# Kernel tuning notes

Measured on AMD Instinct MI355X. Metric: run time of the kernel, lower is better.

The kernel has to match this reference:

```python
import jax, jax.numpy as jnp
import numpy as np

ALPHA = 3.0
NITERS = 15
POWER_ITERS = 20
ROOTS = [np.cos(np.pi * (2 * i + 1) / (2 * NITERS)) for i in range(NITERS)]


def batch_conv2d(inputs, kernels):
    # inputs: [B,1,H,W], kernels: [B,1,3,3]; per-sample 3x3 stencil via grouped conv
    B, _, H, W = inputs.shape
    out = jax.lax.conv_general_dilated(
        inputs.reshape(1, B, H, W), kernels,
        window_strides=(1, 1), padding=((1, 1), (1, 1)),
        feature_group_count=B,
        dimension_numbers=("NCHW", "OIHW", "NCHW"))
    return out.reshape(B, 1, H, W)


def setup_inputs() -> dict:
    key = jax.random.key(0)
    k1, k2, k3, k4 = jax.random.split(key, 4)
    B, H, W = 64, 512, 512
    x = jax.random.normal(k1, (B, 1, H, W), dtype=jnp.float32)
    f = jax.random.normal(k2, (B, 1, H, W), dtype=jnp.float32)
    kernelA = jax.random.normal(k3, (B, 1, 3, 3), dtype=jnp.float32)
    u = jax.random.normal(k4, (B, 1, H, W), dtype=jnp.float32)
    return {"x": x, "f": f, "kernelA": kernelA, "u": u}


def reference(x, f, kernelA, u):
    # Power iteration to estimate the dominant eigenvalue magnitude m per sample
    for _ in range(POWER_ITERS):
        y = batch_conv2d(u, kernelA)
        m = jnp.max(jnp.abs(y), axis=(2, 3), keepdims=True)  # [B,1,1,1]
        u = y / m
    # Chebyshev step sizes over the band [m/alpha, m]
    taus = jnp.stack(
        [2.0 / (m + m / ALPHA - (m / ALPHA - m) * r) for r in ROOTS])  # [niters,B,1,1,1]

    def cheby_step(xc, tau):
        Ax = batch_conv2d(xc, kernelA)
        return xc + tau * (f - Ax), None

    x, _ = jax.lax.scan(cheby_step, x, taus)
    return x
```

## Files before the change

kernel.cpp:

```cpp
#include <hip/hip_runtime.h>

#define BB 64
#define HH 512
#define WW 512
#define PLANE (HH * WW)
#define N_CHEBY 15
#define FD 5
#define RR 32
#define NS (HH / RR)

struct F8 { float v[8]; };

__device__ __forceinline__ float wshr1(float x) {
    return __int_as_float(__builtin_amdgcn_update_dpp(
        0, __float_as_int(x), 0x138, 0xF, 0xF, true));
}
__device__ __forceinline__ float wshl1(float x) {
    return __int_as_float(__builtin_amdgcn_update_dpp(
        0, __float_as_int(x), 0x130, 0xF, 0xF, true));
}

__device__ __forceinline__ F8 ldrow(const float* plane, int y, int lane, bool ok) {
    F8 r;
    if (ok) {
        const float4* p =
            reinterpret_cast<const float4*>(plane + (size_t)y * WW + (lane << 3));
        const float4 a = p[0], b = p[1];
        r.v[0] = a.x; r.v[1] = a.y; r.v[2] = a.z; r.v[3] = a.w;
        r.v[4] = b.x; r.v[5] = b.y; r.v[6] = b.z; r.v[7] = b.w;
    } else {
#pragma unroll
        for (int i = 0; i < 8; ++i) r.v[i] = 0.f;
    }
    return r;
}

__device__ __forceinline__ void racc8(const F8& r, float k0, float k1, float k2,
                                      float acc[8]) {
    const float lf = wshr1(r.v[7]);
    const float rt = wshl1(r.v[0]);
    acc[0] = fmaf(k0, lf, fmaf(k1, r.v[0], fmaf(k2, r.v[1], acc[0])));
#pragma unroll
    for (int c = 1; c < 7; ++c)
        acc[c] = fmaf(k0, r.v[c-1], fmaf(k1, r.v[c], fmaf(k2, r.v[c+1], acc[c])));
    acc[7] = fmaf(k0, r.v[6], fmaf(k1, r.v[7], fmaf(k2, rt, acc[7])));
}

template<int FDv>
__global__ __launch_bounds__(256, 1) void conv_waveT(
    const float* __restrict__ in, const float* __restrict__ kern,
    const float* __restrict__ pm_prev, float* __restrict__ out,
    float* __restrict__ pmw, float* __restrict__ pmz)
{
    constexpr int STEPSv = RR + 2 * FDv;
    const int lane = threadIdx.x & 63;
    const int wid  = threadIdx.x >> 6;
    const int b = blockIdx.y;
    const int stripe = (blockIdx.x << 2) + wid;
    const int ytop = stripe * RR;

    float invv = 1.f;
    if (pm_prev) {
        float v = (lane < NS) ? pm_prev[b * NS + lane] : 0.f;
#pragma unroll
        for (int o = 32; o; o >>= 1) v = fmaxf(v, __shfl_xor(v, o, 64));
        invv = 1.f / v;
    }

    const float* kb = kern + b * 9;
    const float k00=kb[0],k01=kb[1],k02=kb[2],k10=kb[3],k11=kb[4],k12=kb[5],
                k20=kb[6],k21=kb[7],k22=kb[8];
    const float* ip = in + (size_t)b * PLANE;
    float* op = out ? out + (size_t)b * PLANE : nullptr;

    F8 u2 = {}, u1 = {};
    F8 lt[FDv - 1] = {}, lm[FDv - 1] = {};
    float mz = 0.f, mw = 0.f;
    F8 u0 = ldrow(ip, ytop - FDv, lane, (unsigned)(ytop - FDv) < HH);

#pragma unroll 2
    for (int p = 0; p < STEPSv; ++p) {
        const int yL = ytop - FDv + p;
        F8 un = ldrow(ip, yL + 1, lane,
                      (p < STEPSv - 1) && ((unsigned)(yL + 1) < HH));

        F8 nw[FDv - 1];
        {
            float acc[8] = {0,0,0,0,0,0,0,0};
            racc8(u2, k00,k01,k02, acc);
            racc8(u1, k10,k11,k12, acc);
            racc8(u0, k20,k21,k22, acc);
            const int y = yL - 1;
            const bool act = (y >= ytop - (FDv-1)) && (y <= ytop + RR + FDv - 2)
                          && ((unsigned)y < HH);
#pragma unroll
            for (int c = 0; c < 8; ++c) nw[0].v[c] = act ? acc[c] * invv : 0.f;
        }
#pragma unroll
        for (int j = 2; j <= FDv; ++j) {
            float acc[8] = {0,0,0,0,0,0,0,0};
            racc8(lt[j-2], k00,k01,k02, acc);
            racc8(lm[j-2], k10,k11,k12, acc);
            racc8(nw[j-2], k20,k21,k22, acc);
            const int y = yL - j;
            if (j < FDv) {
                const bool act = (y >= ytop - (FDv-j)) && (y <= ytop + RR + FDv - j - 1)
                              && ((unsigned)y < HH);
#pragma unroll
                for (int c = 0; c < 8; ++c) nw[j-1].v[c] = act ? acc[c] : 0.f;
                if (j == FDv - 1) {
#pragma unroll
                    for (int c = 0; c < 8; ++c)
                        mz = fmaxf(mz, fabsf(nw[j-1].v[c]));
                }
            } else {
                if (y >= ytop && y < ytop + RR) {
#pragma unroll
                    for (int c = 0; c < 8; ++c) mw = fmaxf(mw, fabsf(acc[c]));
                    if (op) {
                        float4* q = reinterpret_cast<float4*>(
                            op + (size_t)y * WW + (lane << 3));
                        q[0] = make_float4(acc[0], acc[1], acc[2], acc[3]);
                        q[1] = make_float4(acc[4], acc[5], acc[6], acc[7]);
                    }
                }
            }
        }
#pragma unroll
        for (int l = 0; l < FDv - 1; ++l) { lt[l] = lm[l]; lm[l] = nw[l]; }
        u2 = u1; u1 = u0; u0 = un;
    }

#pragma unroll
    for (int o = 32; o; o >>= 1) {
        mz = fmaxf(mz, __shfl_xor(mz, o, 64));
        mw = fmaxf(mw, __shfl_xor(mw, o, 64));
    }
    if (lane == 0) {
        pmz[b * NS + stripe] = mz;
        pmw[b * NS + stripe] = mw;
    }
}

__global__ __launch_bounds__(64) void tau_k(
    const float* __restrict__ pmz, const float* __restrict__ pmw,
    float* __restrict__ taus)
{
    const int b = blockIdx.x, t = threadIdx.x;
    float vz = (t < NS) ? pmz[b * NS + t] : 0.f;
    float vw = (t < NS) ? pmw[b * NS + t] : 0.f;
#pragma unroll
    for (int o = 32; o; o >>= 1) {
        vz = fmaxf(vz, __shfl_xor(vz, o, 64));
        vw = fmaxf(vw, __shfl_xor(vw, o, 64));
    }
    if (t < N_CHEBY) {
        const float m = vw / vz;
        const double rr = cos(M_PI * (2.0 * t + 1.0) / (2.0 * N_CHEBY));
        const float denom = m + m / 3.0f - (m / 3.0f - m) * (float)rr;
        taus[t * BB + b] = 2.0f / denom;
    }
}

template<int RRv>
__global__ __launch_bounds__(256, 2) void cheby_wave2(
    const float* __restrict__ xin, const float* __restrict__ fin,
    const float* __restrict__ kern, const float* __restrict__ tauv,
    float* __restrict__ xout)
{
    constexpr int STEPSv = RRv + 2 * FD;
    __shared__ float fring[4][FD + 1][8][64];
    const int lane = threadIdx.x & 63;
    const int wid  = threadIdx.x >> 6;
    const int b = blockIdx.y;
    const int stripe = (blockIdx.x << 2) + wid;
    const int ytop = stripe * RRv;
    float (*fr)[8][64] = fring[wid];

    const float* kb = kern + b * 9;
    const float k00=kb[0],k01=kb[1],k02=kb[2],k10=kb[3],k11=kb[4],k12=kb[5],
                k20=kb[6],k21=kb[7],k22=kb[8];
    float tau[FD];
#pragma unroll
    for (int j = 0; j < FD; ++j) tau[j] = tauv[j * BB + b];

    const float* xp = xin + (size_t)b * PLANE;
    const float* fp = fin + (size_t)b * PLANE;
    float* op = xout + (size_t)b * PLANE;

    F8 u2 = {}, u1 = {};
    F8 lt[FD - 1] = {}, lm[FD - 1] = {};
    F8 u0 = ldrow(xp, ytop - FD, lane, (unsigned)(ytop - FD) < HH);

#pragma unroll 2
    for (int p = 0; p < STEPSv; ++p) {
        const int yL = ytop - FD + p;
        F8 un = ldrow(xp, yL + 1, lane,
                      (p < STEPSv - 1) && ((unsigned)(yL + 1) < HH));
        F8 fn = ldrow(fp, yL, lane, (p < STEPSv - 1) && ((unsigned)yL < HH));

        F8 ft[FD];
#pragma unroll
        for (int j = 1; j <= FD; ++j) {
            const int sp = (p + (FD + 1) - j) % (FD + 1);
#pragma unroll
            for (int c = 0; c < 8; ++c) ft[j-1].v[c] = fr[sp][c][lane];
        }

        F8 nw[FD - 1];
        {
            float acc[8] = {0,0,0,0,0,0,0,0};
            racc8(u2, k00,k01,k02, acc);
            racc8(u1, k10,k11,k12, acc);
            racc8(u0, k20,k21,k22, acc);
            const int y = yL - 1;
            const bool act = (y >= ytop - (FD-1)) && (y <= ytop + RRv + FD - 2)
                          && ((unsigned)y < HH);
#pragma unroll
            for (int c = 0; c < 8; ++c)
                nw[0].v[c] = act ? fmaf(tau[0], ft[0].v[c] - acc[c], u1.v[c]) : 0.f;
        }
#pragma unroll
        for (int j = 2; j <= FD; ++j) {
            float acc[8] = {0,0,0,0,0,0,0,0};
            racc8(lt[j-2], k00,k01,k02, acc);
            racc8(lm[j-2], k10,k11,k12, acc);
            racc8(nw[j-2], k20,k21,k22, acc);
            const int y = yL - j;
            if (j < FD) {
                const bool act = (y >= ytop - (FD-j)) && (y <= ytop + RRv + FD - j - 1)
                              && ((unsigned)y < HH);
#pragma unroll
                for (int c = 0; c < 8; ++c)
                    nw[j-1].v[c] =
                        act ? fmaf(tau[j-1], ft[j-1].v[c] - acc[c], lm[j-2].v[c])
                            : 0.f;
            } else {
                if (y >= ytop && y < ytop + RRv) {
                    float4* q = reinterpret_cast<float4*>(
                        op + (size_t)y * WW + (lane << 3));
                    float o0 = fmaf(tau[FD-1], ft[FD-1].v[0] - acc[0], lm[j-2].v[0]);
                    float o1 = fmaf(tau[FD-1], ft[FD-1].v[1] - acc[1], lm[j-2].v[1]);
                    float o2 = fmaf(tau[FD-1], ft[FD-1].v[2] - acc[2], lm[j-2].v[2]);
                    float o3 = fmaf(tau[FD-1], ft[FD-1].v[3] - acc[3], lm[j-2].v[3]);
                    q[0] = make_float4(o0, o1, o2, o3);
                    o0 = fmaf(tau[FD-1], ft[FD-1].v[4] - acc[4], lm[j-2].v[4]);
                    o1 = fmaf(tau[FD-1], ft[FD-1].v[5] - acc[5], lm[j-2].v[5]);
                    o2 = fmaf(tau[FD-1], ft[FD-1].v[6] - acc[6], lm[j-2].v[6]);
                    o3 = fmaf(tau[FD-1], ft[FD-1].v[7] - acc[7], lm[j-2].v[7]);
                    q[1] = make_float4(o0, o1, o2, o3);
                }
            }
        }

        if (p < STEPSv - 1) {
            const int sp = p % (FD + 1);
#pragma unroll
            for (int c = 0; c < 8; ++c) fr[sp][c][lane] = fn.v[c];
        }

#pragma unroll
        for (int l = 0; l < FD - 1; ++l) { lt[l] = lm[l]; lm[l] = nw[l]; }
        u2 = u1; u1 = u0; u0 = un;
    }
}

extern "C" void kernel_launch(void* const* d_in, const int* in_sizes, int n_in,
                              void* d_out, int out_size, void* d_ws, size_t ws_size,
                              hipStream_t stream)
{
    const float* x_in = (const float*)d_in[0];
    const float* f_in = (const float*)d_in[1];
    const float* k_in = (const float*)d_in[2];
    const float* u_in = (const float*)d_in[3];
    float* out = (float*)d_out;

    float* bufA = (float*)d_ws;
    float* pmW0 = bufA + (size_t)BB * PLANE;
    float* pmW1 = pmW0 + BB * NS;
    float* pmZ  = pmW1 + BB * NS;
    float* taus = pmZ  + BB * NS;

    dim3 blk(256);
    dim3 grdc(NS / 4, BB);

    conv_waveT<7><<<grdc, blk, 0, stream>>>(u_in, k_in, nullptr, bufA, pmW0, pmZ);
    conv_waveT<7><<<grdc, blk, 0, stream>>>(bufA, k_in, pmW0, out,  pmW1, pmZ);
    conv_waveT<6><<<grdc, blk, 0, stream>>>(out,  k_in, pmW1, nullptr, pmW0, pmZ);

    tau_k<<<BB, 64, 0, stream>>>(pmZ, pmW0, taus);

    dim3 grdy((HH / 16) / 4, BB);
    cheby_wave2<16><<<grdy, blk, 0, stream>>>(x_in, f_in, k_in, taus,          out);
    cheby_wave2<16><<<grdy, blk, 0, stream>>>(out,  f_in, k_in, taus + 5 * BB, bufA);
    cheby_wave2<16><<<grdy, blk, 0, stream>>>(bufA, f_in, k_in, taus + 10 * BB, out);
}
```

Baseline: 350.9 us.

## Use 16-row stripes and 4 launches of 5-step power-iteration fusion

The power-iteration stage now processes 16-row stripes instead of 32-row stripes, doubling the grid and allowing two blocks per CU via launch bounds. Temporal fusion depth drops from 7/7/6 to 5 per launch, so four launches cover the 20 iterations instead of three. This trades more halo recomputation per stripe (relative to stripe height) and an extra launch and plane round-trip for better occupancy and lower register pressure. The tau kernel is generalized to take the stripe count.

```diff
diff --git a/kernel.cpp b/kernel.cpp
--- a/kernel.cpp
+++ b/kernel.cpp
@@ -6,8 +6,6 @@
 #define PLANE (HH * WW)
 #define N_CHEBY 15
 #define FD 5
-#define RR 32
-#define NS (HH / RR)
 
 struct F8 { float v[8]; };
 
@@ -46,22 +44,23 @@
     acc[7] = fmaf(k0, r.v[6], fmaf(k1, r.v[7], fmaf(k2, rt, acc[7])));
 }
 
-template<int FDv>
-__global__ __launch_bounds__(256, 1) void conv_waveT(
+template<int FDv, int RRv>
+__global__ __launch_bounds__(256, 2) void conv_waveT(
     const float* __restrict__ in, const float* __restrict__ kern,
     const float* __restrict__ pm_prev, float* __restrict__ out,
     float* __restrict__ pmw, float* __restrict__ pmz)
 {
-    constexpr int STEPSv = RR + 2 * FDv;
+    constexpr int NSv = HH / RRv;
+    constexpr int STEPSv = RRv + 2 * FDv;
     const int lane = threadIdx.x & 63;
     const int wid  = threadIdx.x >> 6;
     const int b = blockIdx.y;
     const int stripe = (blockIdx.x << 2) + wid;
-    const int ytop = stripe * RR;
+    const int ytop = stripe * RRv;
 
     float invv = 1.f;
     if (pm_prev) {
-        float v = (lane < NS) ? pm_prev[b * NS + lane] : 0.f;
+        float v = (lane < NSv) ? pm_prev[b * NSv + lane] : 0.f;
 #pragma unroll
         for (int o = 32; o; o >>= 1) v = fmaxf(v, __shfl_xor(v, o, 64));
         invv = 1.f / v;
@@ -91,7 +90,7 @@
             racc8(u1, k10,k11,k12, acc);
             racc8(u0, k20,k21,k22, acc);
             const int y = yL - 1;
-            const bool act = (y >= ytop - (FDv-1)) && (y <= ytop + RR + FDv - 2)
+            const bool act = (y >= ytop - (FDv-1)) && (y <= ytop + RRv + FDv - 2)
                           && ((unsigned)y < HH);
 #pragma unroll
             for (int c = 0; c < 8; ++c) nw[0].v[c] = act ? acc[c] * invv : 0.f;
@@ -104,7 +103,7 @@
             racc8(nw[j-2], k20,k21,k22, acc);
             const int y = yL - j;
             if (j < FDv) {
-                const bool act = (y >= ytop - (FDv-j)) && (y <= ytop + RR + FDv - j - 1)
+                const bool act = (y >= ytop - (FDv-j)) && (y <= ytop + RRv + FDv - j - 1)
                               && ((unsigned)y < HH);
 #pragma unroll
                 for (int c = 0; c < 8; ++c) nw[j-1].v[c] = act ? acc[c] : 0.f;
@@ -114,7 +113,7 @@
                         mz = fmaxf(mz, fabsf(nw[j-1].v[c]));
                 }
             } else {
-                if (y >= ytop && y < ytop + RR) {
+                if (y >= ytop && y < ytop + RRv) {
 #pragma unroll
                     for (int c = 0; c < 8; ++c) mw = fmaxf(mw, fabsf(acc[c]));
                     if (op) {
@@ -137,18 +136,18 @@
         mw = fmaxf(mw, __shfl_xor(mw, o, 64));
     }
     if (lane == 0) {
-        pmz[b * NS + stripe] = mz;
-        pmw[b * NS + stripe] = mw;
+        pmz[b * NSv + stripe] = mz;
+        pmw[b * NSv + stripe] = mw;
     }
 }
 
 __global__ __launch_bounds__(64) void tau_k(
     const float* __restrict__ pmz, const float* __restrict__ pmw,
-    float* __restrict__ taus)
+    float* __restrict__ taus, int n)
 {
     const int b = blockIdx.x, t = threadIdx.x;
-    float vz = (t < NS) ? pmz[b * NS + t] : 0.f;
-    float vw = (t < NS) ? pmw[b * NS + t] : 0.f;
+    float vz = (t < n) ? pmz[b * n + t] : 0.f;
+    float vw = (t < n) ? pmw[b * n + t] : 0.f;
 #pragma unroll
     for (int o = 32; o; o >>= 1) {
         vz = fmaxf(vz, __shfl_xor(vz, o, 64));
@@ -275,20 +274,22 @@
     const float* u_in = (const float*)d_in[3];
     float* out = (float*)d_out;
 
+    constexpr int NSC = HH / 16;
     float* bufA = (float*)d_ws;
     float* pmW0 = bufA + (size_t)BB * PLANE;
-    float* pmW1 = pmW0 + BB * NS;
-    float* pmZ  = pmW1 + BB * NS;
-    float* taus = pmZ  + BB * NS;
+    float* pmW1 = pmW0 + BB * NSC;
+    float* pmZ  = pmW1 + BB * NSC;
+    float* taus = pmZ  + BB * NSC;
 
     dim3 blk(256);
-    dim3 grdc(NS / 4, BB);
-
-    conv_waveT<7><<<grdc, blk, 0, stream>>>(u_in, k_in, nullptr, bufA, pmW0, pmZ);
-    conv_waveT<7><<<grdc, blk, 0, stream>>>(bufA, k_in, pmW0, out,  pmW1, pmZ);
-    conv_waveT<6><<<grdc, blk, 0, stream>>>(out,  k_in, pmW1, nullptr, pmW0, pmZ);
-
-    tau_k<<<BB, 64, 0, stream>>>(pmZ, pmW0, taus);
+    dim3 grdc(NSC / 4, BB);
+
+    conv_waveT<5, 16><<<grdc, blk, 0, stream>>>(u_in, k_in, nullptr, bufA, pmW0, pmZ);
+    conv_waveT<5, 16><<<grdc, blk, 0, stream>>>(bufA, k_in, pmW0, out,  pmW1, pmZ);
+    conv_waveT<5, 16><<<grdc, blk, 0, stream>>>(out,  k_in, pmW1, bufA, pmW0, pmZ);
+    conv_waveT<5, 16><<<grdc, blk, 0, stream>>>(bufA, k_in, pmW0, nullptr, pmW1, pmZ);
+
+    tau_k<<<BB, 64, 0, stream>>>(pmZ, pmW1, taus, NSC);
 
     dim3 grdy((HH / 16) / 4, BB);
     cheby_wave2<16><<<grdy, blk, 0, stream>>>(x_in, f_in, k_in, taus,          out);
```

After: 356.6 us. About the same (+1.6%).
